# Performance work log

Hardware: AMD Instinct MI355X
Metric: run time of the kernel (lower is better)

Reference implementation:

```python
import jax, jax.numpy as jnp
import numpy as np

H = 1024  # hidden size


def lstm_layer(x, W_ih, W_hh, b_ih, b_hh):
    # x: [B, T, in] -> outputs [B, T, H]; torch gate order (i, f, g, o)
    xg = jnp.einsum('bti,gi->btg', x, W_ih) + (b_ih + b_hh)  # [B, T, 4H]
    xg = jnp.swapaxes(xg, 0, 1)  # [T, B, 4H] for scan over time
    B = x.shape[0]
    h0 = jnp.zeros((B, H), x.dtype)
    c0 = jnp.zeros((B, H), x.dtype)

    def step(carry, xg_t):
        h, c = carry
        g = xg_t + h @ W_hh.T  # [B, 4H]
        i, f, gc, o = jnp.split(g, 4, axis=-1)
        i = jax.nn.sigmoid(i)
        f = jax.nn.sigmoid(f)
        gc = jnp.tanh(gc)
        o = jax.nn.sigmoid(o)
        c = f * c + i * gc
        h = o * jnp.tanh(c)
        return (h, c), h

    (_, _), hs = jax.lax.scan(step, (h0, c0), xg)
    return jnp.swapaxes(hs, 0, 1)  # [B, T, H]


def setup_inputs() -> dict:
    key = jax.random.key(0)
    ks = jax.random.split(key, 11)
    s = 1.0 / np.sqrt(H)  # torch LSTM init scale
    return {
        'x': jax.random.normal(ks[0], (64, 512, 128), jnp.float32),
        'W_ih0': jax.random.normal(ks[1], (4 * H, 128), jnp.float32) * s,
        'W_hh0': jax.random.normal(ks[2], (4 * H, H), jnp.float32) * s,
        'b_ih0': jax.random.normal(ks[3], (4 * H,), jnp.float32) * s,
        'b_hh0': jax.random.normal(ks[4], (4 * H,), jnp.float32) * s,
        'W_ih1': jax.random.normal(ks[5], (4 * H, H), jnp.float32) * s,
        'W_hh1': jax.random.normal(ks[6], (4 * H, H), jnp.float32) * s,
        'b_ih1': jax.random.normal(ks[7], (4 * H,), jnp.float32) * s,
        'b_hh1': jax.random.normal(ks[8], (4 * H,), jnp.float32) * s,
        'fc_w': jax.random.normal(ks[9], (1, H), jnp.float32) * s,
        'fc_b': jax.random.normal(ks[10], (1,), jnp.float32) * s,
    }


def reference(x, W_ih0, W_hh0, b_ih0, b_hh0, W_ih1, W_hh1, b_ih1, b_hh1, fc_w, fc_b):
    h1 = lstm_layer(x, W_ih0, W_hh0, b_ih0, b_hh0)   # [B, T, H]
    h2 = lstm_layer(h1, W_ih1, W_hh1, b_ih1, b_hh1)  # [B, T, H]
    return h2[:, -1, :] @ fc_w.T + fc_b              # [B, 1]
```

## Files before the change

### kernel.cpp

```cpp
#include <hip/hip_runtime.h>
#include <math.h>

#define HDIM 1024
#define BDIM 64
#define TDIM 512
#define KIN  128
#define NBLK 256
#define NTHR 1024
#define FRAME (HDIM * BDIM)

typedef _Float16 f16;
typedef __attribute__((ext_vector_type(2))) _Float16 f16x2;
typedef __attribute__((ext_vector_type(8))) _Float16 f16x8;
typedef __attribute__((ext_vector_type(4))) float f32x4;
typedef __attribute__((ext_vector_type(4))) unsigned u32x4;

#define MFMA16(a, b, c) __builtin_amdgcn_mfma_f32_16x16x32_f16((a), (b), (c), 0, 0, 0)

__device__ __forceinline__ float sigm(float x) { return 1.0f / (1.0f + expf(-x)); }

__device__ __forceinline__ f16x8 ld_cg(const f16* p) {
    f16x8 r;
    asm volatile("global_load_dwordx4 %0, %1, off sc0 sc1"
                 : "=v"(r) : "v"(p) : "memory");
    return r;
}
#define VM_WAIT8(r0, r1, r2, r3, r4, r5, r6, r7)                         \
    asm volatile("s_waitcnt vmcnt(0)"                                    \
                 : "+v"(r0), "+v"(r1), "+v"(r2), "+v"(r3),               \
                   "+v"(r4), "+v"(r5), "+v"(r6), "+v"(r7))

__device__ __forceinline__ void st_cg8(f16* p, uint2 v) {
    asm volatile("global_store_dwordx2 %0, %1, off sc0 sc1"
                 :: "v"(p), "v"(v) : "memory");
}
#define VM_DRAIN() asm volatile("s_waitcnt vmcnt(0)" ::: "memory")

__device__ __forceinline__ void tag_pub(unsigned* tag, unsigned v) {
    asm volatile("global_store_dword %0, %1, off sc0 sc1"
                 :: "v"(tag), "v"(v) : "memory");
}
__device__ __forceinline__ void tag_poll(const unsigned* tags, int lane,
                                         unsigned tgt) {
    const unsigned* p = tags + lane * 4;
    for (;;) {
        u32x4 t;
        asm volatile("global_load_dwordx4 %0, %1, off sc0 sc1\n\t"
                     "s_waitcnt vmcnt(0)"
                     : "=v"(t) : "v"(p) : "memory");
        bool ok = (t.x >= tgt) && (t.y >= tgt) && (t.z >= tgt) && (t.w >= tgt);
        if (__all(ok)) break;
        __builtin_amdgcn_s_sleep(1);
    }
}

__global__ void cvt_w(const float* __restrict__ src, f16* __restrict__ dst, int n2) {
    int i = blockIdx.x * blockDim.x + threadIdx.x;
    if (i < n2) {
        float2 a = ((const float2*)src)[i];
        f16x2 o = {(f16)a.x, (f16)a.y};
        ((f16x2*)dst)[i] = o;
    }
}

__global__ void cvt_x(const float* __restrict__ x, f16* __restrict__ xP) {
    int P = blockIdx.x * blockDim.x + threadIdx.x;
    if (P >= TDIM * BDIM * (KIN / 2)) return;
    int kp = P & 63;
    int b  = (P >> 6) & 63;
    int t  = P >> 12;
    float2 v = ((const float2*)x)[((size_t)b * TDIM + t) * (KIN / 2) + kp];
    f16x2 o = {(f16)v.x, (f16)v.y};
    ((f16x2*)xP)[((size_t)t * BDIM + b) * (KIN / 2) + kp] = o;
}

__global__ void __launch_bounds__(NTHR, 4) lstm_fused(
    const f16* __restrict__ xP,
    const f16* __restrict__ Wc0, const f16* __restrict__ Wh0,
    const float* __restrict__ bih0, const float* __restrict__ bhh0,
    const f16* __restrict__ Wc1, const f16* __restrict__ Wh1,
    const float* __restrict__ bih1, const float* __restrict__ bhh1,
    f16* ring1, f16* ring2, unsigned* tagA, unsigned* tagB) {

    __shared__ float red[32 * 324 + 16];
    __shared__ __align__(16) f16 hbuf1[BDIM * 4];
    __shared__ __align__(16) f16 hbuf2[BDIM * 4];

    const int tid  = threadIdx.x;
    const int lane = tid & 63;
    const int w    = __builtin_amdgcn_readfirstlane(tid >> 6);
    const int bid  = (int)blockIdx.x;
    const int iu4  = __builtin_amdgcn_readfirstlane(bid * 4);

    const int n    = lane & 15;
    const int quad = lane >> 4;
    const int am   = lane & 15;
    const int wrow = iu4 + (n >> 2) + (n & 3) * HDIM;

    const int oct4 = iu4 >> 3;
    const int coff = iu4 & 7;

    f16x8 B1x;
    f16x8 B1h[2], B2i[2], B2h[2];
    {
        const int kq = quad * 8;
        if (w < 4)
            B1x = *(const f16x8*)(Wc0 + (size_t)wrow * KIN + w * 32 + kq);
        #pragma unroll
        for (int j = 0; j < 2; ++j) {
            const int ks = (2 * w + j) * 32 + kq;
            B1h[j] = *(const f16x8*)(Wh0 + (size_t)wrow * HDIM + ks);
            B2i[j] = *(const f16x8*)(Wc1 + (size_t)wrow * HDIM + ks);
            B2h[j] = *(const f16x8*)(Wh1 + (size_t)wrow * HDIM + ks);
        }
    }

    float bias1[4], bias2[4];
    float c1 = 0.f, c2 = 0.f;
    const int il = w;
    const int m  = lane;
    if (w < 4) {
        const int i = iu4 + il;
        #pragma unroll
        for (int g = 0; g < 4; ++g) {
            bias1[g] = bih0[i + g * HDIM] + bhh0[i + g * HDIM];
            bias2[g] = bih1[i + g * HDIM] + bhh1[i + g * HDIM];
        }
    }

    if (w == 8) {
        uint2 z = {0u, 0u};
        st_cg8(ring1 + FRAME + oct4 * 512 + lane * 8 + coff, z);
        VM_DRAIN();
        if (lane == 0) tag_pub(tagA + bid, 1u);
    }
    if (w == 9) {
        uint2 z = {0u, 0u};
        st_cg8(ring2 + FRAME + oct4 * 512 + lane * 8 + coff, z);
        VM_DRAIN();
        if (lane == 0) tag_pub(tagB + bid, 1u);
    }

    for (int s = 0; s <= TDIM; ++s) {
        const f16* r1p = ring1 + (size_t)((s + 1) & 1) * FRAME;
        const f16* r2p = ring2 + (size_t)(s & 1) * FRAME;

        if (w == 0) tag_poll(tagA, lane, (unsigned)(s + 1));
        __syncthreads();

        f16x8 A1[2][4];
        #pragma unroll
        for (int j = 0; j < 2; ++j) {
            const int oct = (2 * w + j) * 4 + quad;
            #pragma unroll
            for (int mt = 0; mt < 4; ++mt)
                A1[j][mt] = ld_cg(r1p + oct * 512 + (mt * 16 + am) * 8);
        }
        VM_WAIT8(A1[0][0], A1[0][1], A1[0][2], A1[0][3],
                 A1[1][0], A1[1][1], A1[1][2], A1[1][3]);

        f32x4 acc[4], acc2[4];
        #pragma unroll
        for (int mt = 0; mt < 4; ++mt) {
            acc[mt]  = (f32x4){0.f, 0.f, 0.f, 0.f};
            acc2[mt] = (f32x4){0.f, 0.f, 0.f, 0.f};
        }
        #pragma unroll
        for (int j = 0; j < 2; ++j)
            #pragma unroll
            for (int mt = 0; mt < 4; ++mt) {
                acc[mt]  = MFMA16(A1[j][mt], B1h[j], acc[mt]);
                acc2[mt] = MFMA16(A1[j][mt], B2i[j], acc2[mt]);
            }
        if (w < 4) {
            const int ts = (s < TDIM) ? s : (TDIM - 1);
            const f16* xb = xP + (size_t)ts * BDIM * KIN;
            const int kx = w * 32 + quad * 8;
            #pragma unroll
            for (int mt = 0; mt < 4; ++mt) {
                f16x8 ax = *(const f16x8*)(xb + (size_t)(mt * 16 + am) * KIN + kx);
                acc[mt] = MFMA16(ax, B1x, acc[mt]);
            }
        }

        const int p = w & 7;
        if (w < 8) {
            #pragma unroll
            for (int mt = 0; mt < 4; ++mt)
                *(f32x4*)&red[(p * 4 + mt) * 324 + n * 20 + quad * 4] = acc[mt];
        }
        __syncthreads();
        if (w >= 8) {
            #pragma unroll
            for (int mt = 0; mt < 4; ++mt) {
                float* a = &red[(p * 4 + mt) * 324 + n * 20 + quad * 4];
                f32x4 v = *(f32x4*)a;
                *(f32x4*)a = v + acc[mt];
            }
        }
        __syncthreads();

        if (w < 4 && s < TDIM) {
            const int mt = m >> 4, qm = m & 15;
            float g4[4];
            #pragma unroll
            for (int g = 0; g < 4; ++g) {
                float sum = bias1[g];
                #pragma unroll
                for (int pp = 0; pp < 8; ++pp)
                    sum += red[(pp * 4 + mt) * 324 + (il * 4 + g) * 20 + qm];
                g4[g] = sum;
            }
            float ig = sigm(g4[0]), fg = sigm(g4[1]);
            float gg = tanhf(g4[2]), og = sigm(g4[3]);
            c1 = fg * c1 + ig * gg;
            hbuf1[m * 4 + il] = (f16)(og * tanhf(c1));
        }
        if (w == 15) tag_poll(tagB, lane, (unsigned)s);
        __syncthreads();

        if (w == 8 && s < TDIM) {
            uint2 v = *(const uint2*)&hbuf1[lane * 4];
            st_cg8(ring1 + (size_t)(s & 1) * FRAME + oct4 * 512 + lane * 8 + coff, v);
            VM_DRAIN();
            if (lane == 0) tag_pub(tagA + bid, (unsigned)(s + 2));
        }

        f16x8 A2[2][4];
        #pragma unroll
        for (int j = 0; j < 2; ++j) {
            const int oct = (2 * w + j) * 4 + quad;
            #pragma unroll
            for (int mt = 0; mt < 4; ++mt)
                A2[j][mt] = ld_cg(r2p + oct * 512 + (mt * 16 + am) * 8);
        }
        VM_WAIT8(A2[0][0], A2[0][1], A2[0][2], A2[0][3],
                 A2[1][0], A2[1][1], A2[1][2], A2[1][3]);
        #pragma unroll
        for (int j = 0; j < 2; ++j)
            #pragma unroll
            for (int mt = 0; mt < 4; ++mt)
                acc2[mt] = MFMA16(A2[j][mt], B2h[j], acc2[mt]);

        if (w < 8) {
            #pragma unroll
            for (int mt = 0; mt < 4; ++mt)
                *(f32x4*)&red[(p * 4 + mt) * 324 + n * 20 + quad * 4] = acc2[mt];
        }
        __syncthreads();
        if (w >= 8) {
            #pragma unroll
            for (int mt = 0; mt < 4; ++mt) {
                float* a = &red[(p * 4 + mt) * 324 + n * 20 + quad * 4];
                f32x4 v = *(f32x4*)a;
                *(f32x4*)a = v + acc2[mt];
            }
        }
        __syncthreads();

        if (w < 4 && s >= 1) {
            const int mt = m >> 4, qm = m & 15;
            float g4[4];
            #pragma unroll
            for (int g = 0; g < 4; ++g) {
                float sum = bias2[g];
                #pragma unroll
                for (int pp = 0; pp < 8; ++pp)
                    sum += red[(pp * 4 + mt) * 324 + (il * 4 + g) * 20 + qm];
                g4[g] = sum;
            }
            float ig = sigm(g4[0]), fg = sigm(g4[1]);
            float gg = tanhf(g4[2]), og = sigm(g4[3]);
            c2 = fg * c2 + ig * gg;
            hbuf2[m * 4 + il] = (f16)(og * tanhf(c2));
        }
        __syncthreads();

        if (w == 9 && s >= 1) {
            uint2 v = *(const uint2*)&hbuf2[lane * 4];
            st_cg8(ring2 + (size_t)((s + 1) & 1) * FRAME + oct4 * 512 + lane * 8 + coff, v);
            VM_DRAIN();
            if (lane == 0) tag_pub(tagB + bid, (unsigned)(s + 1));
        }
    }
}

__global__ void fc_kernel(const f16* __restrict__ h2f,
                          const float* __restrict__ fcw,
                          const float* __restrict__ fcb,
                          float* __restrict__ out) {
    __shared__ float red[256];
    const int tid = threadIdx.x;
    const int b = tid >> 2, q = tid & 3;
    float s = 0.f;
    for (int oct = q * 32; oct < (q + 1) * 32; ++oct) {
        f16x8 v = *(const f16x8*)(h2f + oct * 512 + b * 8);
        #pragma unroll
        for (int j = 0; j < 8; ++j)
            s = fmaf((float)v[j], fcw[oct * 8 + j], s);
    }
    red[tid] = s;
    __syncthreads();
    if (q == 0)
        out[b] = red[tid] + red[tid + 1] + red[tid + 2] + red[tid + 3] + fcb[0];
}

extern "C" void kernel_launch(void* const* d_in, const int* in_sizes, int n_in,
                              void* d_out, int out_size, void* d_ws, size_t ws_size,
                              hipStream_t stream) {
    const float* x    = (const float*)d_in[0];
    const float* Wih0 = (const float*)d_in[1];
    const float* Whh0 = (const float*)d_in[2];
    const float* bih0 = (const float*)d_in[3];
    const float* bhh0 = (const float*)d_in[4];
    const float* Wih1 = (const float*)d_in[5];
    const float* Whh1 = (const float*)d_in[6];
    const float* bih1 = (const float*)d_in[7];
    const float* bhh1 = (const float*)d_in[8];
    const float* fcw  = (const float*)d_in[9];
    const float* fcb  = (const float*)d_in[10];
    float* out = (float*)d_out;

    f16* xPd   = (f16*)d_ws;
    f16* Wc0   = xPd + (size_t)TDIM * BDIM * KIN;
    f16* Wh0   = Wc0 + (size_t)4 * HDIM * KIN;
    f16* Wc1   = Wh0 + (size_t)4 * HDIM * HDIM;
    f16* Wh1   = Wc1 + (size_t)4 * HDIM * HDIM;
    f16* ring1 = Wh1 + (size_t)4 * HDIM * HDIM;
    f16* ring2 = ring1 + 2 * FRAME;
    unsigned* tagA = (unsigned*)(ring2 + 2 * FRAME);
    unsigned* tagB = tagA + 512;

    hipMemsetAsync(tagA, 0, 4096, stream);
    {
        int n2 = 4 * HDIM * KIN / 2;
        cvt_w<<<dim3((n2 + 255) / 256), dim3(256), 0, stream>>>(Wih0, Wc0, n2);
        n2 = 4 * HDIM * HDIM / 2;
        cvt_w<<<dim3((n2 + 255) / 256), dim3(256), 0, stream>>>(Whh0, Wh0, n2);
        cvt_w<<<dim3((n2 + 255) / 256), dim3(256), 0, stream>>>(Whh1, Wh1, n2);
        cvt_w<<<dim3((n2 + 255) / 256), dim3(256), 0, stream>>>(Wih1, Wc1, n2);
    }
    {
        int np = TDIM * BDIM * (KIN / 2);
        cvt_x<<<dim3((np + 255) / 256), dim3(256), 0, stream>>>(x, xPd);
    }

    void* args[13];
    args[0]  = (void*)&xPd;
    args[1]  = (void*)&Wc0;
    args[2]  = (void*)&Wh0;
    args[3]  = (void*)&bih0;
    args[4]  = (void*)&bhh0;
    args[5]  = (void*)&Wc1;
    args[6]  = (void*)&Wh1;
    args[7]  = (void*)&bih1;
    args[8]  = (void*)&bhh1;
    args[9]  = (void*)&ring1;
    args[10] = (void*)&ring2;
    args[11] = (void*)&tagA;
    args[12] = (void*)&tagB;
    hipLaunchCooperativeKernel(reinterpret_cast<void*>(lstm_fused), dim3(NBLK), dim3(NTHR),
                               args, 0, stream);

    fc_kernel<<<dim3(1), dim3(256), 0, stream>>>(ring2 + FRAME, fcw, fcb, out);
}
```

Baseline: 3.039 ms.

## Split batch across two block groups, each block owning eight hidden units

Work is repartitioned so each of the 256 blocks computes 8 hidden units for half the batch (32 rows) instead of 4 units for all 64 rows. The ring buffer layout becomes two batch sub-frames, and the fc kernel indexing changes to match. Each block now reads half as much h state per step from global memory and reuses each A fragment across two weight tiles. In exchange it holds twice the weight registers, and each tag poll only needs the 128 blocks sharing a batch half, though polling still scans all tags.

```diff
diff --git a/kernel.cpp b/kernel.cpp
--- a/kernel.cpp
+++ b/kernel.cpp
@@ -8,6 +8,7 @@
 #define NBLK 256
 #define NTHR 1024
 #define FRAME (HDIM * BDIM)
+#define SUBF  (HDIM * 32)
 
 typedef _Float16 f16;
 typedef __attribute__((ext_vector_type(2))) _Float16 f16x2;
@@ -25,10 +26,9 @@
                  : "=v"(r) : "v"(p) : "memory");
     return r;
 }
-#define VM_WAIT8(r0, r1, r2, r3, r4, r5, r6, r7)                         \
+#define VM_WAIT4(r0, r1, r2, r3)                                         \
     asm volatile("s_waitcnt vmcnt(0)"                                    \
-                 : "+v"(r0), "+v"(r1), "+v"(r2), "+v"(r3),               \
-                   "+v"(r4), "+v"(r5), "+v"(r6), "+v"(r7))
+                 : "+v"(r0), "+v"(r1), "+v"(r2), "+v"(r3))
 
 __device__ __forceinline__ void st_cg8(f16* p, uint2 v) {
     asm volatile("global_store_dwordx2 %0, %1, off sc0 sc1"
@@ -83,44 +83,58 @@
     f16* ring1, f16* ring2, unsigned* tagA, unsigned* tagB) {
 
     __shared__ float red[32 * 324 + 16];
-    __shared__ __align__(16) f16 hbuf1[BDIM * 4];
-    __shared__ __align__(16) f16 hbuf2[BDIM * 4];
+    __shared__ __align__(16) f16 hbuf1[32 * 8];
+    __shared__ __align__(16) f16 hbuf2[32 * 8];
 
     const int tid  = threadIdx.x;
     const int lane = tid & 63;
     const int w    = __builtin_amdgcn_readfirstlane(tid >> 6);
     const int bid  = (int)blockIdx.x;
-    const int iu4  = __builtin_amdgcn_readfirstlane(bid * 4);
+    const int cg   = __builtin_amdgcn_readfirstlane(bid & 127);
+    const int bg   = __builtin_amdgcn_readfirstlane(bid >> 7);
+    const int i0   = cg * 8;
+    const int b0   = bg * 32;
 
     const int n    = lane & 15;
     const int quad = lane >> 4;
     const int am   = lane & 15;
-    const int wrow = iu4 + (n >> 2) + (n & 3) * HDIM;
-
-    const int oct4 = iu4 >> 3;
-    const int coff = iu4 & 7;
-
-    f16x8 B1x;
-    f16x8 B1h[2], B2i[2], B2h[2];
+    const int kq   = quad * 8;
+
+    int wr[2];
+    #pragma unroll
+    for (int nt = 0; nt < 2; ++nt)
+        wr[nt] = i0 + nt * 4 + (n >> 2) + (n & 3) * HDIM;
+
+    f16x8 B1x[2];
+    f16x8 B1h[2][2], B2i[2][2], B2h[2][2];
     {
-        const int kq = quad * 8;
         if (w < 4)
-            B1x = *(const f16x8*)(Wc0 + (size_t)wrow * KIN + w * 32 + kq);
+            #pragma unroll
+            for (int nt = 0; nt < 2; ++nt)
+                B1x[nt] = *(const f16x8*)(Wc0 + (size_t)wr[nt] * KIN + w * 32 + kq);
         #pragma unroll
         for (int j = 0; j < 2; ++j) {
             const int ks = (2 * w + j) * 32 + kq;
-            B1h[j] = *(const f16x8*)(Wh0 + (size_t)wrow * HDIM + ks);
-            B2i[j] = *(const f16x8*)(Wc1 + (size_t)wrow * HDIM + ks);
-            B2h[j] = *(const f16x8*)(Wh1 + (size_t)wrow * HDIM + ks);
+            #pragma unroll
+            for (int nt = 0; nt < 2; ++nt) {
+                B1h[j][nt] = *(const f16x8*)(Wh0 + (size_t)wr[nt] * HDIM + ks);
+                B2i[j][nt] = *(const f16x8*)(Wc1 + (size_t)wr[nt] * HDIM + ks);
+                B2h[j][nt] = *(const f16x8*)(Wh1 + (size_t)wr[nt] * HDIM + ks);
+            }
         }
     }
 
     float bias1[4], bias2[4];
     float c1 = 0.f, c2 = 0.f;
-    const int il = w;
-    const int m  = lane;
+    const int il   = w;
+    const int cO   = il * 2 + (lane >> 5);
+    const int b32O = lane & 31;
+    const int mtO  = (lane >> 4) & 1;
+    const int qmO  = lane & 15;
+    const int ntO  = il >> 1;
+    const int nbO  = ((il & 1) * 2 + (lane >> 5)) * 4;
     if (w < 4) {
-        const int i = iu4 + il;
+        const int i = i0 + cO;
         #pragma unroll
         for (int g = 0; g < 4; ++g) {
             bias1[g] = bih0[i + g * HDIM] + bhh0[i + g * HDIM];
@@ -130,155 +144,169 @@
 
     if (w == 8) {
         uint2 z = {0u, 0u};
-        st_cg8(ring1 + FRAME + oct4 * 512 + lane * 8 + coff, z);
+        st_cg8(ring1 + FRAME + bg * SUBF + cg * 256 + lane * 4, z);
         VM_DRAIN();
         if (lane == 0) tag_pub(tagA + bid, 1u);
     }
     if (w == 9) {
         uint2 z = {0u, 0u};
-        st_cg8(ring2 + FRAME + oct4 * 512 + lane * 8 + coff, z);
+        st_cg8(ring2 + FRAME + bg * SUBF + cg * 256 + lane * 4, z);
         VM_DRAIN();
         if (lane == 0) tag_pub(tagB + bid, 1u);
     }
 
     for (int s = 0; s <= TDIM; ++s) {
-        const f16* r1p = ring1 + (size_t)((s + 1) & 1) * FRAME;
-        const f16* r2p = ring2 + (size_t)(s & 1) * FRAME;
+        const f16* r1p = ring1 + (size_t)((s + 1) & 1) * FRAME + bg * SUBF;
+        const f16* r2p = ring2 + (size_t)(s & 1) * FRAME + bg * SUBF;
 
         if (w == 0) tag_poll(tagA, lane, (unsigned)(s + 1));
         __syncthreads();
 
-        f16x8 A1[2][4];
+        f16x8 A1[2][2];
         #pragma unroll
         for (int j = 0; j < 2; ++j) {
             const int oct = (2 * w + j) * 4 + quad;
             #pragma unroll
-            for (int mt = 0; mt < 4; ++mt)
-                A1[j][mt] = ld_cg(r1p + oct * 512 + (mt * 16 + am) * 8);
-        }
-        VM_WAIT8(A1[0][0], A1[0][1], A1[0][2], A1[0][3],
-                 A1[1][0], A1[1][1], A1[1][2], A1[1][3]);
-
-        f32x4 acc[4], acc2[4];
-        #pragma unroll
-        for (int mt = 0; mt < 4; ++mt) {
-            acc[mt]  = (f32x4){0.f, 0.f, 0.f, 0.f};
-            acc2[mt] = (f32x4){0.f, 0.f, 0.f, 0.f};
-        }
+            for (int mt = 0; mt < 2; ++mt)
+                A1[j][mt] = ld_cg(r1p + oct * 256 + (mt * 16 + am) * 8);
+        }
+        VM_WAIT4(A1[0][0], A1[0][1], A1[1][0], A1[1][1]);
+
+        f32x4 acc[2][2], acc2[2][2];
+        #pragma unroll
+        for (int mt = 0; mt < 2; ++mt)
+            #pragma unroll
+            for (int nt = 0; nt < 2; ++nt) {
+                acc[mt][nt]  = (f32x4){0.f, 0.f, 0.f, 0.f};
+                acc2[mt][nt] = (f32x4){0.f, 0.f, 0.f, 0.f};
+            }
         #pragma unroll
         for (int j = 0; j < 2; ++j)
             #pragma unroll
-            for (int mt = 0; mt < 4; ++mt) {
-                acc[mt]  = MFMA16(A1[j][mt], B1h[j], acc[mt]);
-                acc2[mt] = MFMA16(A1[j][mt], B2i[j], acc2[mt]);
-            }
+            for (int nt = 0; nt < 2; ++nt)
+                #pragma unroll
+                for (int mt = 0; mt < 2; ++mt) {
+                    acc[mt][nt]  = MFMA16(A1[j][mt], B1h[j][nt], acc[mt][nt]);
+                    acc2[mt][nt] = MFMA16(A1[j][mt], B2i[j][nt], acc2[mt][nt]);
+                }
         if (w < 4) {
             const int ts = (s < TDIM) ? s : (TDIM - 1);
             const f16* xb = xP + (size_t)ts * BDIM * KIN;
-            const int kx = w * 32 + quad * 8;
-            #pragma unroll
-            for (int mt = 0; mt < 4; ++mt) {
-                f16x8 ax = *(const f16x8*)(xb + (size_t)(mt * 16 + am) * KIN + kx);
-                acc[mt] = MFMA16(ax, B1x, acc[mt]);
-            }
+            const int kx = w * 32 + kq;
+            f16x8 ax[2];
+            #pragma unroll
+            for (int mt = 0; mt < 2; ++mt)
+                ax[mt] = *(const f16x8*)(xb + (size_t)(b0 + mt * 16 + am) * KIN + kx);
+            #pragma unroll
+            for (int nt = 0; nt < 2; ++nt)
+                #pragma unroll
+                for (int mt = 0; mt < 2; ++mt)
+                    acc[mt][nt] = MFMA16(ax[mt], B1x[nt], acc[mt][nt]);
         }
 
         const int p = w & 7;
         if (w < 8) {
             #pragma unroll
-            for (int mt = 0; mt < 4; ++mt)
-                *(f32x4*)&red[(p * 4 + mt) * 324 + n * 20 + quad * 4] = acc[mt];
+            for (int mt = 0; mt < 2; ++mt)
+                #pragma unroll
+                for (int nt = 0; nt < 2; ++nt)
+                    *(f32x4*)&red[(p * 4 + mt * 2 + nt) * 324 + n * 20 + quad * 4] = acc[mt][nt];
         }
         __syncthreads();
         if (w >= 8) {
             #pragma unroll
-            for (int mt = 0; mt < 4; ++mt) {
-                float* a = &red[(p * 4 + mt) * 324 + n * 20 + quad * 4];
-                f32x4 v = *(f32x4*)a;
-                *(f32x4*)a = v + acc[mt];
-            }
+            for (int mt = 0; mt < 2; ++mt)
+                #pragma unroll
+                for (int nt = 0; nt < 2; ++nt) {
+                    float* a = &red[(p * 4 + mt * 2 + nt) * 324 + n * 20 + quad * 4];
+                    f32x4 v = *(f32x4*)a;
+                    *(f32x4*)a = v + acc[mt][nt];
+                }
         }
         __syncthreads();
 
         if (w < 4 && s < TDIM) {
-            const int mt = m >> 4, qm = m & 15;
             float g4[4];
             #pragma unroll
             for (int g = 0; g < 4; ++g) {
                 float sum = bias1[g];
                 #pragma unroll
                 for (int pp = 0; pp < 8; ++pp)
-                    sum += red[(pp * 4 + mt) * 324 + (il * 4 + g) * 20 + qm];
+                    sum += red[(pp * 4 + mtO * 2 + ntO) * 324 + (nbO + g) * 20 + qmO];
                 g4[g] = sum;
             }
             float ig = sigm(g4[0]), fg = sigm(g4[1]);
             float gg = tanhf(g4[2]), og = sigm(g4[3]);
             c1 = fg * c1 + ig * gg;
-            hbuf1[m * 4 + il] = (f16)(og * tanhf(c1));
+            hbuf1[b32O * 8 + cO] = (f16)(og * tanhf(c1));
         }
         if (w == 15) tag_poll(tagB, lane, (unsigned)s);
         __syncthreads();
 
         if (w == 8 && s < TDIM) {
             uint2 v = *(const uint2*)&hbuf1[lane * 4];
-            st_cg8(ring1 + (size_t)(s & 1) * FRAME + oct4 * 512 + lane * 8 + coff, v);
+            st_cg8(ring1 + (size_t)(s & 1) * FRAME + bg * SUBF + cg * 256 + lane * 4, v);
             VM_DRAIN();
             if (lane == 0) tag_pub(tagA + bid, (unsigned)(s + 2));
         }
 
-        f16x8 A2[2][4];
+        f16x8 A2[2][2];
         #pragma unroll
         for (int j = 0; j < 2; ++j) {
             const int oct = (2 * w + j) * 4 + quad;
             #pragma unroll
-            for (int mt = 0; mt < 4; ++mt)
-                A2[j][mt] = ld_cg(r2p + oct * 512 + (mt * 16 + am) * 8);
-        }
-        VM_WAIT8(A2[0][0], A2[0][1], A2[0][2], A2[0][3],
-                 A2[1][0], A2[1][1], A2[1][2], A2[1][3]);
+            for (int mt = 0; mt < 2; ++mt)
+                A2[j][mt] = ld_cg(r2p + oct * 256 + (mt * 16 + am) * 8);
+        }
+        VM_WAIT4(A2[0][0], A2[0][1], A2[1][0], A2[1][1]);
         #pragma unroll
         for (int j = 0; j < 2; ++j)
             #pragma unroll
-            for (int mt = 0; mt < 4; ++mt)
-                acc2[mt] = MFMA16(A2[j][mt], B2h[j], acc2[mt]);
+            for (int nt = 0; nt < 2; ++nt)
+                #pragma unroll
+                for (int mt = 0; mt < 2; ++mt)
+                    acc2[mt][nt] = MFMA16(A2[j][mt], B2h[j][nt], acc2[mt][nt]);
 
         if (w < 8) {
             #pragma unroll
-            for (int mt = 0; mt < 4; ++mt)
-                *(f32x4*)&red[(p * 4 + mt) * 324 + n * 20 + quad * 4] = acc2[mt];
+            for (int mt = 0; mt < 2; ++mt)
+                #pragma unroll
+                for (int nt = 0; nt < 2; ++nt)
+                    *(f32x4*)&red[(p * 4 + mt * 2 + nt) * 324 + n * 20 + quad * 4] = acc2[mt][nt];
         }
         __syncthreads();
         if (w >= 8) {
             #pragma unroll
-            for (int mt = 0; mt < 4; ++mt) {
-                float* a = &red[(p * 4 + mt) * 324 + n * 20 + quad * 4];
-                f32x4 v = *(f32x4*)a;
-                *(f32x4*)a = v + acc2[mt];
-            }
+            for (int mt = 0; mt < 2; ++mt)
+                #pragma unroll
+                for (int nt = 0; nt < 2; ++nt) {
+                    float* a = &red[(p * 4 + mt * 2 + nt) * 324 + n * 20 + quad * 4];
+                    f32x4 v = *(f32x4*)a;
+                    *(f32x4*)a = v + acc2[mt][nt];
+                }
         }
         __syncthreads();
 
         if (w < 4 && s >= 1) {
-            const int mt = m >> 4, qm = m & 15;
             float g4[4];
             #pragma unroll
             for (int g = 0; g < 4; ++g) {
                 float sum = bias2[g];
                 #pragma unroll
                 for (int pp = 0; pp < 8; ++pp)
-                    sum += red[(pp * 4 + mt) * 324 + (il * 4 + g) * 20 + qm];
+                    sum += red[(pp * 4 + mtO * 2 + ntO) * 324 + (nbO + g) * 20 + qmO];
                 g4[g] = sum;
             }
             float ig = sigm(g4[0]), fg = sigm(g4[1]);
             float gg = tanhf(g4[2]), og = sigm(g4[3]);
             c2 = fg * c2 + ig * gg;
-            hbuf2[m * 4 + il] = (f16)(og * tanhf(c2));
+            hbuf2[b32O * 8 + cO] = (f16)(og * tanhf(c2));
         }
         __syncthreads();
 
         if (w == 9 && s >= 1) {
             uint2 v = *(const uint2*)&hbuf2[lane * 4];
-            st_cg8(ring2 + (size_t)((s + 1) & 1) * FRAME + oct4 * 512 + lane * 8 + coff, v);
+            st_cg8(ring2 + (size_t)((s + 1) & 1) * FRAME + bg * SUBF + cg * 256 + lane * 4, v);
             VM_DRAIN();
             if (lane == 0) tag_pub(tagB + bid, (unsigned)(s + 1));
         }
@@ -292,9 +320,10 @@
     __shared__ float red[256];
     const int tid = threadIdx.x;
     const int b = tid >> 2, q = tid & 3;
+    const int base = (b >> 5) * SUBF + (b & 31) * 8;
     float s = 0.f;
     for (int oct = q * 32; oct < (q + 1) * 32; ++oct) {
-        f16x8 v = *(const f16x8*)(h2f + oct * 512 + b * 8);
+        f16x8 v = *(const f16x8*)(h2f + base + oct * 256);
         #pragma unroll
         for (int j = 0; j < 8; ++j)
             s = fmaf((float)v[j], fcw[oct * 8 + j], s);
```

Result: slower. 3.158 ms (+3.9%).
